# Optimization experiments

Hardware: AMD Instinct MI355X
Metric: run time of the kernel (lower is better)

Reference implementation:

```python
import jax, jax.numpy as jnp
import numpy as np

D = 1024
H = 16
HD = D // H
SCALE = HD ** -0.5


def setup_inputs() -> dict:
    key = jax.random.key(0)
    ks = jax.random.split(key, 6)
    B, S = 2, 2048
    lim = np.sqrt(6.0 / (D + D))  # xavier uniform for square weights
    query = jax.random.normal(ks[0], (B, S, D), dtype=jnp.float32)
    Wq = jax.random.uniform(ks[1], (D, D), jnp.float32, -lim, lim)
    Wk = jax.random.uniform(ks[2], (D, D), jnp.float32, -lim, lim)
    Wv = jax.random.uniform(ks[3], (D, D), jnp.float32, -lim, lim)
    Wo = jax.random.uniform(ks[4], (D, D), jnp.float32, -lim, lim)
    bq = jnp.zeros((D,), jnp.float32)
    bk = jnp.zeros((D,), jnp.float32)
    bv = jnp.zeros((D,), jnp.float32)
    bo = jnp.zeros((D,), jnp.float32)
    # causal mask: True = masked (strictly upper triangular)
    attn_mask = jnp.triu(jnp.ones((S, S), dtype=bool), k=1)
    return {"query": query, "Wq": Wq, "bq": bq, "Wk": Wk, "bk": bk,
            "Wv": Wv, "bv": bv, "Wo": Wo, "bo": bo, "attn_mask": attn_mask}


def reference(query, Wq, bq, Wk, bk, Wv, bv, Wo, bo, attn_mask):
    B, Sq, _ = query.shape
    # projections (torch Linear: x @ W.T + b); self-attention (key=value=query)
    q = (query @ Wq.T + bq).reshape(B, Sq, H, HD).transpose(0, 2, 1, 3)  # [B,H,Sq,hd]
    k = (query @ Wk.T + bk).reshape(B, Sq, H, HD).transpose(0, 2, 1, 3)
    v = (query @ Wv.T + bv).reshape(B, Sq, H, HD).transpose(0, 2, 1, 3)
    scores = jnp.einsum('bhqd,bhkd->bhqk', q, k) * SCALE
    scores = jnp.where(attn_mask[None, None, :, :], -jnp.inf, scores)
    weights = jax.nn.softmax(scores, axis=-1)  # dropout p=0.0 -> identity
    out = jnp.einsum('bhqk,bhkd->bhqd', weights, v)
    out = out.transpose(0, 2, 1, 3).reshape(B, Sq, D)
    output = out @ Wo.T + bo
    return output, weights
```

## Files before the change

kernel.cpp:

```cpp
#include <hip/hip_runtime.h>
#include <hip/hip_bf16.h>
#include <stdint.h>

#define DMODEL 1024
#define NH     16
#define HDIM   64
#define BATCH  2
#define SEQ    2048
#define NROWS  (BATCH*SEQ)
#define NBH    (BATCH*NH)
#define SCALE  0.125f

typedef unsigned short u16;
typedef __bf16 bf16x8 __attribute__((ext_vector_type(8)));
typedef float  f32x4  __attribute__((ext_vector_type(4)));

#define MFMA(a,b,c) __builtin_amdgcn_mfma_f32_16x16x32_bf16((a),(b),(c),0,0,0)
#define BAR() __builtin_amdgcn_s_barrier()
#define WAITVM(N) asm volatile("s_waitcnt vmcnt(" #N ")" ::: "memory")

__device__ __forceinline__ u16 f2bf(float f) {
  union { float f; uint32_t u; } v; v.f = f;
  return (u16)((v.u + 0x7fffu + ((v.u >> 16) & 1u)) >> 16);
}

__device__ __forceinline__ void gl16(const void* g, void* l) {
  __builtin_amdgcn_global_load_lds((const __attribute__((address_space(1))) void*)g,
                                   (__attribute__((address_space(3))) void*)l,
                                   16, 0, 0);
}

#define LDF(arr, r, ch) (*(const bf16x8*)(&(arr)[(((r) << 6)) + ((((ch) ^ ((r) & 7))) << 3)]))
#define LDV(r, ch)      (*(const bf16x8*)(&lv [(((r) << 7)) + ((((ch) ^ ((r) & 7))) << 3)]))

#define XCH   (NROWS*DMODEL/4)
#define WCH   (DMODEL*DMODEL/4)
__global__ void cvt_all(const float* __restrict__ x,  const float* __restrict__ Wq,
                        const float* __restrict__ Wk, const float* __restrict__ Wv,
                        const float* __restrict__ Wo,
                        u16* __restrict__ Xb, u16* __restrict__ Wqb, u16* __restrict__ Wkb,
                        u16* __restrict__ Wvb, u16* __restrict__ Wob)
{
  int g = blockIdx.x * 256 + threadIdx.x;
  const float* src; u16* dst; int off;
  if (g < XCH) { src = x; dst = Xb; off = g * 4; }
  else {
    int t = g - XCH; int w = t >> 18; off = (t & (WCH - 1)) * 4;
    src = (w == 0) ? Wq : (w == 1) ? Wk : (w == 2) ? Wv : Wo;
    dst = (w == 0) ? Wqb : (w == 1) ? Wkb : (w == 2) ? Wvb : Wob;
  }
  float4 f = *(const float4*)(src + off);
  ushort4 o;
  o.x = f2bf(f.x); o.y = f2bf(f.y); o.z = f2bf(f.z); o.w = f2bf(f.w);
  *(ushort4*)(dst + off) = o;
}

__launch_bounds__(256, 3)
__global__ void qkv_proj(const u16* __restrict__ Xb,
                         const u16* __restrict__ Wqb,
                         const u16* __restrict__ Wkb,
                         const u16* __restrict__ Wvb,
                         const float* __restrict__ bqp,
                         const float* __restrict__ bkp,
                         const float* __restrict__ bvp,
                         u16* __restrict__ qb, u16* __restrict__ kb, u16* __restrict__ vtb)
{
  __shared__ __attribute__((aligned(16))) u16 la[128 * 64];
  __shared__ __attribute__((aligned(16))) u16 lb[128 * 64];
  const int tid  = threadIdx.x;
  const int lane = tid & 63, wave = tid >> 6;
  const int quad = lane >> 4, lm = lane & 15;

  int flat = blockIdx.y * 32 + blockIdx.x;
  int jj = flat >> 3;
  const int m0 = ((flat & 7) * 4 + (jj & 3)) * 128;
  const int ct = jj >> 2;
  const int proj = ct >> 3;
  const int n0 = (ct & 7) * 128;
  const u16*  W    = (proj == 0) ? Wqb : (proj == 1) ? Wkb : Wvb;
  const float* bias = (proj == 0) ? bqp : (proj == 1) ? bkp : bvp;

  const int sr = tid >> 3, sch = tid & 7;

  const f32x4 fzero = {0.f, 0.f, 0.f, 0.f};
  f32x4 acc[4][4];
#pragma unroll
  for (int i = 0; i < 4; i++)
#pragma unroll
    for (int j = 0; j < 4; j++) acc[i][j] = fzero;

  const int wm0 = (wave & 1) * 64, wn0 = (wave >> 1) * 64;

  for (int k0 = 0; k0 < DMODEL; k0 += 64) {
#pragma unroll
    for (int i = 0; i < 4; i++) {
      int r = sr + i * 32;
      int cs = (sch ^ (r & 7)) << 3;
      gl16(Xb + (size_t)(m0 + r) * DMODEL + k0 + cs, &la[(wave * 64 + i * 256) << 3]);
      gl16(W  + (size_t)(n0 + r) * DMODEL + k0 + cs, &lb[(wave * 64 + i * 256) << 3]);
    }
    WAITVM(0);
    BAR();
#pragma unroll
    for (int ks = 0; ks < 2; ks++) {
      bf16x8 af[4], bfg[4];
#pragma unroll
      for (int i = 0; i < 4; i++) af[i]  = LDF(la, wm0 + i * 16 + lm, ks * 4 + quad);
#pragma unroll
      for (int j = 0; j < 4; j++) bfg[j] = LDF(lb, wn0 + j * 16 + lm, ks * 4 + quad);
#pragma unroll
      for (int i = 0; i < 4; i++)
#pragma unroll
        for (int j = 0; j < 4; j++)
          acc[i][j] = MFMA(af[i], bfg[j], acc[i][j]);
    }
    BAR();
  }

#pragma unroll
  for (int j = 0; j < 4; j++) {
    int o = n0 + wn0 + j * 16 + lm;
    float bs = bias[o];
    int h = o >> 6, hd = o & 63;
#pragma unroll
    for (int i = 0; i < 4; i++) {
      int m = m0 + wm0 + i * 16 + quad * 4;
      int b = m >> 11, ss = m & (SEQ - 1);
      if (proj == 2) {
        ushort4 ov;
        ov.x = f2bf(acc[i][j][0] + bs); ov.y = f2bf(acc[i][j][1] + bs);
        ov.z = f2bf(acc[i][j][2] + bs); ov.w = f2bf(acc[i][j][3] + bs);
        *(ushort4*)(vtb + (((size_t)(b * NH + h)) * HDIM + hd) * SEQ + ss) = ov;
      } else {
        u16* dst = (proj == 0) ? qb : kb;
#pragma unroll
        for (int r = 0; r < 4; r++)
          dst[(((size_t)(b * NH + h)) * SEQ + ss + r) * HDIM + hd] = f2bf(acc[i][j][r] + bs);
      }
    }
  }
}

__launch_bounds__(256, 3)
__global__ void attn_fused(const u16* __restrict__ qb, const u16* __restrict__ kb,
                           const u16* __restrict__ vtb,
                           float* __restrict__ wts, u16* __restrict__ ctxb)
{
  __shared__ __attribute__((aligned(16))) u16 lk[128 * 64];
  __shared__ __attribute__((aligned(16))) u16 lv[64 * 128];
  __shared__ __attribute__((aligned(16))) u16 lp[4][16 * 128];

  const int tid  = threadIdx.x;
  const int lane = tid & 63, wave = tid >> 6;
  const int quad = lane >> 4, lm = lane & 15;

  int flat = blockIdx.x;
  int wk = (flat & 7) * 128 + (flat >> 3);
  const int bh = wk >> 5;
  const int qt = 31 - (wk & 31);
  const int b = bh >> 4, hh = bh & 15;
  u16* lpw = lp[wave];

  const u16* Qb = qb  + (size_t)bh * SEQ * HDIM;
  const u16* K  = kb  + (size_t)bh * SEQ * HDIM;
  const u16* Vt = vtb + (size_t)bh * HDIM * SEQ;

  const f32x4 fzero = {0.f, 0.f, 0.f, 0.f};
  const int kr0 = tid >> 3, kch = tid & 7;
  const int vr0 = tid >> 4, vch = tid & 15;

  const int ktmax = qt >> 1;
  const int qg = qt * 64 + wave * 16 + lm;
  float* Wr = wts + ((size_t)bh * SEQ + qt * 64) * SEQ;

  bf16x8 qreg0 = *(const bf16x8*)(Qb + (size_t)(qt * 64 + wave * 16 + lm) * HDIM + (quad << 3));
  bf16x8 qreg1 = *(const bf16x8*)(Qb + (size_t)(qt * 64 + wave * 16 + lm) * HDIM + 32 + (quad << 3));

  float lsum = 0.f;
#pragma unroll 1
  for (int kt = 0; kt <= ktmax; kt++) {
#pragma unroll
    for (int i = 0; i < 4; i++) {
      int r = kr0 + i * 32;
      gl16(K + (size_t)(kt * 128 + r) * HDIM + ((kch ^ (r & 7)) << 3),
           &lk[(wave * 64 + i * 256) << 3]);
    }
    WAITVM(0);
    BAR();
    f32x4 s[8];
#pragma unroll
    for (int t = 0; t < 8; t++) s[t] = fzero;
    __builtin_amdgcn_s_setprio(1);
#pragma unroll
    for (int t = 0; t < 8; t++) {
      int rr = t * 16 + lm;
      s[t] = MFMA(LDF(lk, rr, quad),     qreg0, s[t]);
      s[t] = MFMA(LDF(lk, rr, 4 + quad), qreg1, s[t]);
    }
    __builtin_amdgcn_s_setprio(0);
#pragma unroll
    for (int t = 0; t < 8; t++)
#pragma unroll
      for (int r = 0; r < 4; r++) {
        int kc = kt * 128 + t * 16 + quad * 4 + r;
        lsum += (kc <= qg) ? __expf(s[t][r] * SCALE) : 0.f;
      }
    BAR();
  }
  lsum += __shfl_xor(lsum, 16);
  lsum += __shfl_xor(lsum, 32);
  const float linv = 1.f / lsum;

  f32x4 acc_o[4];
#pragma unroll
  for (int dt = 0; dt < 4; dt++) acc_o[dt] = fzero;

#pragma unroll 1
  for (int kt = 0; kt <= ktmax; kt++) {
#pragma unroll
    for (int i = 0; i < 4; i++) {
      int r = kr0 + i * 32;
      gl16(K + (size_t)(kt * 128 + r) * HDIM + ((kch ^ (r & 7)) << 3),
           &lk[(wave * 64 + i * 256) << 3]);
    }
#pragma unroll
    for (int i = 0; i < 4; i++) {
      int r = vr0 + i * 16;
      gl16(Vt + (size_t)r * SEQ + kt * 128 + ((vch ^ (r & 7)) << 3),
           &lv[(wave * 64 + i * 256) << 3]);
    }
    WAITVM(0);
    BAR();

    f32x4 s[8];
#pragma unroll
    for (int t = 0; t < 8; t++) s[t] = fzero;
    __builtin_amdgcn_s_setprio(1);
#pragma unroll
    for (int t = 0; t < 8; t++) {
      int rr = t * 16 + lm;
      s[t] = MFMA(LDF(lk, rr, quad),     qreg0, s[t]);
      s[t] = MFMA(LDF(lk, rr, 4 + quad), qreg1, s[t]);
    }
    __builtin_amdgcn_s_setprio(0);

#pragma unroll
    for (int t = 0; t < 8; t++) {
      f32x4 pv;
#pragma unroll
      for (int r = 0; r < 4; r++) {
        int kc = kt * 128 + t * 16 + quad * 4 + r;
        float p = __expf(s[t][r] * SCALE) * linv;
        pv[r] = (kc <= qg) ? p : 0.f;
      }
      *(f32x4*)(Wr + (size_t)(wave * 16 + lm) * SEQ + kt * 128 + t * 16 + quad * 4) = pv;
      ushort4 pb4;
      pb4.x = f2bf(pv[0]); pb4.y = f2bf(pv[1]); pb4.z = f2bf(pv[2]); pb4.w = f2bf(pv[3]);
      int c8 = (t * 4 + quad) ^ ((lm & 7) << 1);
      *(ushort4*)(lpw + lm * 128 + (c8 << 2)) = pb4;
    }

    __builtin_amdgcn_s_setprio(1);
#pragma unroll
    for (int ks = 0; ks < 4; ks++) {
      int c8r = (ks * 8 + quad * 2) ^ ((lm & 7) << 1);
      bf16x8 pb = *(const bf16x8*)(lpw + lm * 128 + (c8r << 2));
#pragma unroll
      for (int dt = 0; dt < 4; dt++) {
        bf16x8 a = LDV(dt * 16 + lm, ks * 4 + quad);
        acc_o[dt] = MFMA(a, pb, acc_o[dt]);
      }
    }
    __builtin_amdgcn_s_setprio(0);
    BAR();
  }

  const int kz = (ktmax + 1) * 128;
  if (kz < SEQ) {
#pragma unroll
    for (int rg = 0; rg < 4; rg++) {
      float* rp = Wr + (size_t)(wave * 16 + rg * 4 + quad) * SEQ;
      for (int c = kz + lm * 4; c < SEQ; c += 64)
        *(f32x4*)(rp + c) = fzero;
    }
  }

  {
    int q = qt * 64 + wave * 16 + lm;
    u16* cp = ctxb + ((size_t)(b * SEQ + q)) * DMODEL + hh * HDIM;
#pragma unroll
    for (int dt = 0; dt < 4; dt++) {
      ushort4 o;
      o.x = f2bf(acc_o[dt][0]); o.y = f2bf(acc_o[dt][1]);
      o.z = f2bf(acc_o[dt][2]); o.w = f2bf(acc_o[dt][3]);
      *(ushort4*)(cp + dt * 16 + quad * 4) = o;
    }
  }
}

__launch_bounds__(256, 3)
__global__ void out_proj(const u16* __restrict__ ctxb, const u16* __restrict__ Wob,
                         const float* __restrict__ bop, float* __restrict__ out)
{
  __shared__ __attribute__((aligned(16))) u16 la[128 * 64];
  __shared__ __attribute__((aligned(16))) u16 lb[128 * 64];
  const int tid  = threadIdx.x;
  const int lane = tid & 63, wave = tid >> 6;
  const int quad = lane >> 4, lm = lane & 15;

  int flat = blockIdx.y * 32 + blockIdx.x;
  int jj = flat >> 3;
  const int m0 = ((flat & 7) * 4 + (jj & 3)) * 128;
  const int n0 = (jj >> 2) * 128;

  const int sr = tid >> 3, sch = tid & 7;

  const f32x4 fzero = {0.f, 0.f, 0.f, 0.f};
  f32x4 acc[4][4];
#pragma unroll
  for (int i = 0; i < 4; i++)
#pragma unroll
    for (int j = 0; j < 4; j++) acc[i][j] = fzero;

  const int wm0 = (wave & 1) * 64, wn0 = (wave >> 1) * 64;

  for (int k0 = 0; k0 < DMODEL; k0 += 64) {
#pragma unroll
    for (int i = 0; i < 4; i++) {
      int r = sr + i * 32;
      int cs = (sch ^ (r & 7)) << 3;
      gl16(ctxb + (size_t)(m0 + r) * DMODEL + k0 + cs, &la[(wave * 64 + i * 256) << 3]);
      gl16(Wob  + (size_t)(n0 + r) * DMODEL + k0 + cs, &lb[(wave * 64 + i * 256) << 3]);
    }
    WAITVM(0);
    BAR();
#pragma unroll
    for (int ks = 0; ks < 2; ks++) {
      bf16x8 af[4], bfg[4];
#pragma unroll
      for (int i = 0; i < 4; i++) af[i]  = LDF(la, wm0 + i * 16 + lm, ks * 4 + quad);
#pragma unroll
      for (int j = 0; j < 4; j++) bfg[j] = LDF(lb, wn0 + j * 16 + lm, ks * 4 + quad);
#pragma unroll
      for (int i = 0; i < 4; i++)
#pragma unroll
        for (int j = 0; j < 4; j++)
          acc[i][j] = MFMA(af[i], bfg[j], acc[i][j]);
    }
    BAR();
  }

#pragma unroll
  for (int j = 0; j < 4; j++) {
    int o = n0 + wn0 + j * 16 + lm;
    float bs = bop[o];
#pragma unroll
    for (int i = 0; i < 4; i++)
#pragma unroll
      for (int r = 0; r < 4; r++) {
        int m = m0 + wm0 + i * 16 + quad * 4 + r;
        out[(size_t)m * DMODEL + o] = acc[i][j][r] + bs;
      }
  }
}

extern "C" void kernel_launch(void* const* d_in, const int* in_sizes, int n_in,
                              void* d_out, int out_size, void* d_ws, size_t ws_size,
                              hipStream_t stream)
{
  (void)in_sizes; (void)n_in; (void)out_size; (void)ws_size;
  const float* x  = (const float*)d_in[0];
  const float* Wq = (const float*)d_in[1];
  const float* bq = (const float*)d_in[2];
  const float* Wk = (const float*)d_in[3];
  const float* bk = (const float*)d_in[4];
  const float* Wv = (const float*)d_in[5];
  const float* bv = (const float*)d_in[6];
  const float* Wo = (const float*)d_in[7];
  const float* bo = (const float*)d_in[8];

  float* out = (float*)d_out;
  float* wts = out + (size_t)NROWS * DMODEL;

  u16* Xb   = (u16*)d_ws;
  u16* Wqb  = Xb   + (size_t)NROWS * DMODEL;
  u16* Wkb  = Wqb  + (size_t)DMODEL * DMODEL;
  u16* Wvb  = Wkb  + (size_t)DMODEL * DMODEL;
  u16* Wob  = Wvb  + (size_t)DMODEL * DMODEL;
  u16* qb   = Wob  + (size_t)DMODEL * DMODEL;
  u16* kb   = qb   + (size_t)NROWS * DMODEL;
  u16* vtb  = kb   + (size_t)NROWS * DMODEL;
  u16* ctxb = vtb  + (size_t)NROWS * DMODEL;

  cvt_all<<<(XCH + 4 * WCH) / 256, 256, 0, stream>>>(x, Wq, Wk, Wv, Wo,
                                                     Xb, Wqb, Wkb, Wvb, Wob);
  qkv_proj<<<dim3(NROWS / 128, 24), 256, 0, stream>>>(Xb, Wqb, Wkb, Wvb, bq, bk, bv, qb, kb, vtb);
  attn_fused<<<1024, 256, 0, stream>>>(qb, kb, vtb, wts, ctxb);
  out_proj<<<dim3(NROWS / 128, DMODEL / 128), 256, 0, stream>>>(ctxb, Wob, bo, out);
}
```

Measured before the change: 680.1 us.

## Double-buffer K loads, prefetch next K/V tiles, fold scale into Q, skip masks

Moves the softmax scale into the Q projection epilogue, so attention no longer multiplies every score by it. The first pass double-buffers K tiles, reusing the V LDS buffer as the second K buffer. The second pass prefetches the next K tile and V tile while the current tile is being computed, using partial vmcnt waits. The causal-mask compare is now applied only on the last (diagonal) tile. The aim is to hide global-to-LDS load latency and cut ALU work per element, at the cost of more barriers and fragile vmcnt counting, which must also account for the weight stores to global memory.

```diff
diff --git a/kernel.cpp b/kernel.cpp
--- a/kernel.cpp
+++ b/kernel.cpp
@@ -9,7 +9,6 @@
 #define SEQ    2048
 #define NROWS  (BATCH*SEQ)
 #define NBH    (BATCH*NH)
-#define SCALE  0.125f
 
 typedef unsigned short u16;
 typedef __bf16 bf16x8 __attribute__((ext_vector_type(8)));
@@ -117,6 +116,7 @@
     BAR();
   }
 
+  const float sc = (proj == 0) ? 0.125f : 1.0f;
 #pragma unroll
   for (int j = 0; j < 4; j++) {
     int o = n0 + wn0 + j * 16 + lm;
@@ -135,7 +135,7 @@
         u16* dst = (proj == 0) ? qb : kb;
 #pragma unroll
         for (int r = 0; r < 4; r++)
-          dst[(((size_t)(b * NH + h)) * SEQ + ss + r) * HDIM + hd] = f2bf(acc[i][j][r] + bs);
+          dst[(((size_t)(b * NH + h)) * SEQ + ss + r) * HDIM + hd] = f2bf((acc[i][j][r] + bs) * sc);
       }
     }
   }
@@ -176,35 +176,63 @@
   bf16x8 qreg0 = *(const bf16x8*)(Qb + (size_t)(qt * 64 + wave * 16 + lm) * HDIM + (quad << 3));
   bf16x8 qreg1 = *(const bf16x8*)(Qb + (size_t)(qt * 64 + wave * 16 + lm) * HDIM + 32 + (quad << 3));
 
-  float lsum = 0.f;
-#pragma unroll 1
-  for (int kt = 0; kt <= ktmax; kt++) {
+  auto stageK = [&](int kt, u16* dst) {
 #pragma unroll
     for (int i = 0; i < 4; i++) {
       int r = kr0 + i * 32;
       gl16(K + (size_t)(kt * 128 + r) * HDIM + ((kch ^ (r & 7)) << 3),
-           &lk[(wave * 64 + i * 256) << 3]);
-    }
-    WAITVM(0);
-    BAR();
-    f32x4 s[8];
-#pragma unroll
-    for (int t = 0; t < 8; t++) s[t] = fzero;
+           dst + ((wave * 64 + i * 256) << 3));
+    }
+  };
+  auto stageV = [&](int kt) {
+#pragma unroll
+    for (int i = 0; i < 4; i++) {
+      int r = vr0 + i * 16;
+      gl16(Vt + (size_t)r * SEQ + kt * 128 + ((vch ^ (r & 7)) << 3),
+           lv + ((wave * 64 + i * 256) << 3));
+    }
+  };
+  auto qk = [&](const u16* kt_, f32x4* s) {
     __builtin_amdgcn_s_setprio(1);
 #pragma unroll
     for (int t = 0; t < 8; t++) {
       int rr = t * 16 + lm;
-      s[t] = MFMA(LDF(lk, rr, quad),     qreg0, s[t]);
-      s[t] = MFMA(LDF(lk, rr, 4 + quad), qreg1, s[t]);
+      s[t] = MFMA(LDF(kt_, rr, quad),     qreg0, s[t]);
+      s[t] = MFMA(LDF(kt_, rr, 4 + quad), qreg1, s[t]);
     }
     __builtin_amdgcn_s_setprio(0);
-#pragma unroll
-    for (int t = 0; t < 8; t++)
-#pragma unroll
-      for (int r = 0; r < 4; r++) {
-        int kc = kt * 128 + t * 16 + quad * 4 + r;
-        lsum += (kc <= qg) ? __expf(s[t][r] * SCALE) : 0.f;
-      }
+  };
+
+  float lsum = 0.f;
+  stageK(0, lk);
+#pragma unroll 1
+  for (int kt = 0; kt <= ktmax; kt++) {
+    u16* cb = (kt & 1) ? lv : lk;
+    if (kt < ktmax) {
+      stageK(kt + 1, (kt & 1) ? lk : lv);
+      WAITVM(4);
+    } else {
+      WAITVM(0);
+    }
+    BAR();
+    f32x4 s[8];
+#pragma unroll
+    for (int t = 0; t < 8; t++) s[t] = fzero;
+    qk(cb, s);
+    if (kt < ktmax) {
+#pragma unroll
+      for (int t = 0; t < 8; t++)
+#pragma unroll
+        for (int r = 0; r < 4; r++) lsum += __expf(s[t][r]);
+    } else {
+#pragma unroll
+      for (int t = 0; t < 8; t++)
+#pragma unroll
+        for (int r = 0; r < 4; r++) {
+          int kc = kt * 128 + t * 16 + quad * 4 + r;
+          lsum += (kc <= qg) ? __expf(s[t][r]) : 0.f;
+        }
+    }
     BAR();
   }
   lsum += __shfl_xor(lsum, 16);
@@ -215,50 +243,50 @@
 #pragma unroll
   for (int dt = 0; dt < 4; dt++) acc_o[dt] = fzero;
 
+  stageK(0, lk);
+  stageV(0);
+  WAITVM(4);
+  BAR();
 #pragma unroll 1
   for (int kt = 0; kt <= ktmax; kt++) {
-#pragma unroll
-    for (int i = 0; i < 4; i++) {
-      int r = kr0 + i * 32;
-      gl16(K + (size_t)(kt * 128 + r) * HDIM + ((kch ^ (r & 7)) << 3),
-           &lk[(wave * 64 + i * 256) << 3]);
-    }
-#pragma unroll
-    for (int i = 0; i < 4; i++) {
-      int r = vr0 + i * 16;
-      gl16(Vt + (size_t)r * SEQ + kt * 128 + ((vch ^ (r & 7)) << 3),
-           &lv[(wave * 64 + i * 256) << 3]);
-    }
-    WAITVM(0);
-    BAR();
-
     f32x4 s[8];
 #pragma unroll
     for (int t = 0; t < 8; t++) s[t] = fzero;
-    __builtin_amdgcn_s_setprio(1);
-#pragma unroll
-    for (int t = 0; t < 8; t++) {
-      int rr = t * 16 + lm;
-      s[t] = MFMA(LDF(lk, rr, quad),     qreg0, s[t]);
-      s[t] = MFMA(LDF(lk, rr, 4 + quad), qreg1, s[t]);
-    }
-    __builtin_amdgcn_s_setprio(0);
-
-#pragma unroll
-    for (int t = 0; t < 8; t++) {
-      f32x4 pv;
-#pragma unroll
-      for (int r = 0; r < 4; r++) {
-        int kc = kt * 128 + t * 16 + quad * 4 + r;
-        float p = __expf(s[t][r] * SCALE) * linv;
-        pv[r] = (kc <= qg) ? p : 0.f;
+    qk(lk, s);
+    BAR();
+    if (kt < ktmax) stageK(kt + 1, lk);
+
+    if (kt < ktmax) {
+#pragma unroll
+      for (int t = 0; t < 8; t++) {
+        f32x4 pv;
+#pragma unroll
+        for (int r = 0; r < 4; r++) pv[r] = __expf(s[t][r]) * linv;
+        *(f32x4*)(Wr + (size_t)(wave * 16 + lm) * SEQ + kt * 128 + t * 16 + quad * 4) = pv;
+        ushort4 pb4;
+        pb4.x = f2bf(pv[0]); pb4.y = f2bf(pv[1]); pb4.z = f2bf(pv[2]); pb4.w = f2bf(pv[3]);
+        int c8 = (t * 4 + quad) ^ ((lm & 7) << 1);
+        *(ushort4*)(lpw + lm * 128 + (c8 << 2)) = pb4;
       }
-      *(f32x4*)(Wr + (size_t)(wave * 16 + lm) * SEQ + kt * 128 + t * 16 + quad * 4) = pv;
-      ushort4 pb4;
-      pb4.x = f2bf(pv[0]); pb4.y = f2bf(pv[1]); pb4.z = f2bf(pv[2]); pb4.w = f2bf(pv[3]);
-      int c8 = (t * 4 + quad) ^ ((lm & 7) << 1);
-      *(ushort4*)(lpw + lm * 128 + (c8 << 2)) = pb4;
-    }
+      WAITVM(12);
+    } else {
+#pragma unroll
+      for (int t = 0; t < 8; t++) {
+        f32x4 pv;
+#pragma unroll
+        for (int r = 0; r < 4; r++) {
+          int kc = kt * 128 + t * 16 + quad * 4 + r;
+          pv[r] = (kc <= qg) ? __expf(s[t][r]) * linv : 0.f;
+        }
+        *(f32x4*)(Wr + (size_t)(wave * 16 + lm) * SEQ + kt * 128 + t * 16 + quad * 4) = pv;
+        ushort4 pb4;
+        pb4.x = f2bf(pv[0]); pb4.y = f2bf(pv[1]); pb4.z = f2bf(pv[2]); pb4.w = f2bf(pv[3]);
+        int c8 = (t * 4 + quad) ^ ((lm & 7) << 1);
+        *(ushort4*)(lpw + lm * 128 + (c8 << 2)) = pb4;
+      }
+      WAITVM(8);
+    }
+    BAR();
 
     __builtin_amdgcn_s_setprio(1);
 #pragma unroll
@@ -273,6 +301,11 @@
     }
     __builtin_amdgcn_s_setprio(0);
     BAR();
+    if (kt < ktmax) {
+      stageV(kt + 1);
+      WAITVM(12);
+      BAR();
+    }
   }
 
   const int kz = (ktmax + 1) * 128;
```

Measured after the change: 683.8 us. About the same (+0.6%).
